# Optimization experiments

Measured on AMD Instinct MI355X. Metric: run time of the kernel, lower is better.

The kernel has to match this reference:

```python
import jax, jax.numpy as jnp
import numpy as np

EMB = 384
H = 6
D = 64
B = 256
T = 256


def setup_inputs() -> dict:
    key = jax.random.key(0)
    ks = jax.random.split(key, 6)
    s = 1.0 / np.sqrt(EMB)
    return {
        "x": jax.random.normal(ks[0], (B, T, EMB), dtype=jnp.float32),
        "wq": jax.random.normal(ks[1], (H, EMB, D), dtype=jnp.float32) * s,
        "wk": jax.random.normal(ks[2], (H, EMB, D), dtype=jnp.float32) * s,
        "wv": jax.random.normal(ks[3], (H, EMB, D), dtype=jnp.float32) * s,
        "w_proj": jax.random.normal(ks[4], (H * D, EMB), dtype=jnp.float32) * s,
        "b_proj": jax.random.normal(ks[5], (EMB,), dtype=jnp.float32) * 0.01,
    }


def reference(x, wq, wk, wv, w_proj, b_proj):
    # x: [B, T, E]; per-head projections stacked over H (dropout in eval mode)
    q = jnp.einsum("bte,hed->bhtd", x, wq)
    k = jnp.einsum("bte,hed->bhtd", x, wk)
    v = jnp.einsum("bte,hed->bhtd", x, wv)
    scale = q.shape[-1] ** -0.5
    scores = jnp.einsum("bhqd,bhkd->bhqk", q, k) * scale  # [B,H,T,T]
    tq = q.shape[2]
    causal = jnp.tril(jnp.ones((tq, tq), dtype=bool))
    scores = jnp.where(causal, scores, -jnp.inf)
    att = jax.nn.softmax(scores, axis=-1)
    out = jnp.einsum("bhqk,bhkd->bhqd", att, v)  # [B,H,T,D]
    out = out.transpose(0, 2, 1, 3).reshape(x.shape[0], tq, -1)  # concat heads
    return out @ w_proj + b_proj
```

## Files before the change

kernel.cpp:

```cpp
#include <hip/hip_runtime.h>
#include <hip/hip_bf16.h>


#define Bn 256
#define Tn 256
#define En 384
#define Hn 6
#define Dn 64

typedef __bf16 bf16x8 __attribute__((ext_vector_type(8)));
typedef float f32x4 __attribute__((ext_vector_type(4)));
typedef unsigned short u16x8 __attribute__((ext_vector_type(8)));

static __device__ __forceinline__ unsigned short f2bf(float f) {
    unsigned int u = __builtin_bit_cast(unsigned int, f);
    u += 0x7fffu + ((u >> 16) & 1u);
    return (unsigned short)(u >> 16);
}

static __device__ __forceinline__ f32x4 mfma16(bf16x8 a, bf16x8 b, f32x4 c) {
    return __builtin_amdgcn_mfma_f32_16x16x32_bf16(a, b, c, 0, 0, 0);
}

static __device__ __forceinline__ void glds16(const unsigned short* g, unsigned short* l) {
    __builtin_amdgcn_global_load_lds(
        (const __attribute__((address_space(1))) unsigned int*)g,
        (__attribute__((address_space(3))) unsigned int*)l, 16, 0, 0);
}

__global__ __launch_bounds__(256) void prep_kernel(
    const float* __restrict__ wq, const float* __restrict__ wk,
    const float* __restrict__ wv, const float* __restrict__ wp,
    unsigned short* __restrict__ wt, unsigned short* __restrict__ wpt) {
    const int NW = 3 * Hn * Dn * En;
    const int NP = En * En;
    int idx = blockIdx.x * 256 + threadIdx.x;
    if (idx < NW) {
        int e = idx % En;
        int d = (idx / En) % Dn;
        int h = (idx / (En * Dn)) % Hn;
        int t = idx / (En * Dn * Hn);
        const float* src = (t == 0) ? wq : (t == 1) ? wk : wv;
        wt[idx] = f2bf(src[(h * En + e) * Dn + d]);
    } else if (idx < NW + NP) {
        int j = idx - NW;
        int k = j % En;
        int n = j / En;
        wpt[j] = f2bf(wp[k * En + n]);
    }
}

__global__ __launch_bounds__(256) void xcast_kernel(
    const float* __restrict__ x, unsigned short* __restrict__ xb) {
    size_t i = ((size_t)blockIdx.x * 256 + threadIdx.x) * 8;
    float4 f0 = *(const float4*)(x + i);
    float4 f1 = *(const float4*)(x + i + 4);
    u16x8 p;
    p[0] = f2bf(f0.x); p[1] = f2bf(f0.y); p[2] = f2bf(f0.z); p[3] = f2bf(f0.w);
    p[4] = f2bf(f1.x); p[5] = f2bf(f1.y); p[6] = f2bf(f1.z); p[7] = f2bf(f1.w);
    *(u16x8*)(xb + i) = p;
}

__global__ __launch_bounds__(256) void qkv_gemm(
    const unsigned short* __restrict__ xb, const unsigned short* __restrict__ wt,
    unsigned short* __restrict__ Qo, unsigned short* __restrict__ Ko,
    unsigned short* __restrict__ Vt) {
    __shared__ unsigned short As[2][128][64];
    __shared__ unsigned short Bs[2][192][64];

    const int bid = blockIdx.x;
    const int swz = (bid & 7) * 384 + (bid >> 3);
    const int h = swz % Hn;
    const int m0 = (swz / Hn) * 128;

    const int tid = threadIdx.x;
    const int wave = tid >> 6, lane = tid & 63;
    const int quad = lane >> 4, l16 = lane & 15;
    const int mw = (wave >> 1) * 64, nw = (wave & 1) * 96;

    f32x4 acc[4][6];
#pragma unroll
    for (int i = 0; i < 4; ++i)
#pragma unroll
        for (int j = 0; j < 6; ++j) acc[i][j] = (f32x4){0.f, 0.f, 0.f, 0.f};

    const int lr = lane >> 3;
    const int js = (lane & 7) ^ lr;

    const unsigned short* ga[4];
#pragma unroll
    for (int i = 0; i < 4; ++i)
        ga[i] = xb + (size_t)(m0 + wave * 32 + i * 8 + lr) * En + js * 8;
    const unsigned short* gb[6];
#pragma unroll
    for (int i = 0; i < 6; ++i) {
        int n = wave * 48 + i * 8 + lr;
        gb[i] = wt + (size_t)(((n >> 6) * Hn + h) * Dn + (n & 63)) * En + js * 8;
    }

#define QKV_STAGE(buf, koff)                                              \
    do {                                                                  \
        _Pragma("unroll") for (int i = 0; i < 4; ++i)                     \
            glds16(ga[i] + (koff), &As[buf][wave * 32 + i * 8][0]);       \
        _Pragma("unroll") for (int i = 0; i < 6; ++i)                     \
            glds16(gb[i] + (koff), &Bs[buf][wave * 48 + i * 8][0]);       \
    } while (0)

    QKV_STAGE(0, 0);
    QKV_STAGE(1, 64);

#pragma unroll
    for (int kb = 0; kb < 6; ++kb) {
        if (kb < 5) asm volatile("s_waitcnt vmcnt(10)" ::: "memory");
        else        asm volatile("s_waitcnt vmcnt(0)" ::: "memory");
        __builtin_amdgcn_s_barrier();

        const int cur = kb & 1;
#pragma unroll
        for (int ks = 0; ks < 2; ++ks) {
            bf16x8 a[4], b[6];
            const int ps = ((ks * 4 + quad) ^ (l16 & 7)) * 8;
#pragma unroll
            for (int mi = 0; mi < 4; ++mi)
                a[mi] = *(const bf16x8*)&As[cur][mw + mi * 16 + l16][ps];
#pragma unroll
            for (int ni = 0; ni < 6; ++ni)
                b[ni] = *(const bf16x8*)&Bs[cur][nw + ni * 16 + l16][ps];
#pragma unroll
            for (int mi = 0; mi < 4; ++mi)
#pragma unroll
                for (int ni = 0; ni < 6; ++ni) acc[mi][ni] = mfma16(a[mi], b[ni], acc[mi][ni]);
        }

        if (kb < 4) {
            __builtin_amdgcn_s_barrier();
            QKV_STAGE(cur, (kb + 2) * 64);
        }
    }
#undef QKV_STAGE

    const int b = m0 >> 8, tbase = m0 & 255;
    unsigned short* qkbase[2] = {
        Qo + (size_t)((b * Hn + h) * Tn) * Dn,
        Ko + (size_t)((b * Hn + h) * Tn) * Dn };
    unsigned short* vdst = Vt + (size_t)((b * Hn + h) * Dn) * Tn;
#pragma unroll
    for (int ni = 0; ni < 6; ++ni) {
        const int ng = nw + ni * 16;
        const int tensor = ng >> 6;
        const int d = (ng & 63) + l16;
        if (tensor < 2) {
            unsigned short* dst = qkbase[tensor];
#pragma unroll
            for (int mi = 0; mi < 4; ++mi)
#pragma unroll
                for (int r = 0; r < 4; ++r) {
                    int t = tbase + mw + mi * 16 + quad * 4 + r;
                    dst[t * Dn + d] = f2bf(acc[mi][ni][r]);
                }
        } else {
#pragma unroll
            for (int mi = 0; mi < 4; ++mi) {
                int t0 = tbase + mw + mi * 16 + quad * 4;
                ushort4 pk;
                pk.x = f2bf(acc[mi][ni][0]);
                pk.y = f2bf(acc[mi][ni][1]);
                pk.z = f2bf(acc[mi][ni][2]);
                pk.w = f2bf(acc[mi][ni][3]);
                *(ushort4*)&vdst[d * Tn + t0] = pk;
            }
        }
    }
}

__global__ __launch_bounds__(256) void attn_kernel(
    const unsigned short* __restrict__ Q, const unsigned short* __restrict__ K,
    const unsigned short* __restrict__ Vt, unsigned short* __restrict__ attout) {
    __shared__ unsigned short Kt[256][64];
    __shared__ unsigned short Vl[64][256];
    __shared__ unsigned short P[4][16][72];

    const int h = blockIdx.x, b = blockIdx.y;
    const unsigned short* Qb = Q + (size_t)((b * Hn + h) * Tn) * Dn;
    const unsigned short* Kb = K + (size_t)((b * Hn + h) * Tn) * Dn;
    const unsigned short* Vb = Vt + (size_t)((b * Hn + h) * Dn) * Tn;

    const int tid = threadIdx.x;
    const int wave = tid >> 6, lane = tid & 63;
    const int quad = lane >> 4, l16 = lane & 15;

    {
        const unsigned short* kg = Kb + (size_t)(lane >> 3) * Dn + ((lane & 7) ^ (lane >> 3)) * 8;
#pragma unroll
        for (int i = 0; i < 8; ++i) {
            const int c = wave * 8 + i;
            glds16(kg + (size_t)c * 8 * Dn, &Kt[c * 8][0]);
        }
#pragma unroll
        for (int i = 0; i < 8; ++i) {
            const int c = wave * 8 + i;
            const int d = c * 2 + (lane >> 5);
            const int j = (lane & 31) ^ (d & 7);
            glds16(Vb + (size_t)d * Tn + j * 8, &Vl[c * 2][0]);
        }
    }
    __syncthreads();

    const float cexp = 0.125f * 1.44269504f;
    const int grp[4] = {wave, 7 - wave, 8 + wave, 15 - wave};

    for (int gi = 0; gi < 4; ++gi) {
        const int g = grp[gi];
        const int q0 = g * 16;

        bf16x8 aq[2];
#pragma unroll
        for (int ks = 0; ks < 2; ++ks)
            aq[ks] = *(const bf16x8*)&Qb[(q0 + l16) * Dn + ks * 32 + quad * 8];

        f32x4 O[4];
#pragma unroll
        for (int i = 0; i < 4; ++i) O[i] = (f32x4){0.f, 0.f, 0.f, 0.f};
        float rsum[4] = {0.f, 0.f, 0.f, 0.f};

        const int ktmax = g >> 2;
        for (int kt = 0; kt <= ktmax; ++kt) {
            f32x4 S[4];
#pragma unroll
            for (int i = 0; i < 4; ++i) S[i] = (f32x4){0.f, 0.f, 0.f, 0.f};
#pragma unroll
            for (int ks = 0; ks < 2; ++ks)
#pragma unroll
                for (int ni = 0; ni < 4; ++ni) {
                    bf16x8 bk = *(const bf16x8*)
                        &Kt[kt * 64 + ni * 16 + l16][(((ks * 4 + quad) ^ (l16 & 7)) * 8)];
                    S[ni] = mfma16(aq[ks], bk, S[ni]);
                }

#pragma unroll
            for (int ni = 0; ni < 4; ++ni)
#pragma unroll
                for (int r = 0; r < 4; ++r) {
                    int col = kt * 64 + ni * 16 + l16;
                    float p = exp2f(S[ni][r] * cexp);
                    p = (col > q0 + quad * 4 + r) ? 0.f : p;
                    rsum[r] += p;
                    P[wave][quad * 4 + r][ni * 16 + l16] = f2bf(p);
                }

#pragma unroll
            for (int ks = 0; ks < 2; ++ks) {
                bf16x8 ap = *(const bf16x8*)&P[wave][l16][ks * 32 + quad * 8];
#pragma unroll
                for (int ni = 0; ni < 4; ++ni) {
                    bf16x8 bv = *(const bf16x8*)
                        &Vl[ni * 16 + l16][(((kt * 8 + ks * 4 + quad) ^ (l16 & 7)) * 8)];
                    O[ni] = mfma16(ap, bv, O[ni]);
                }
            }
        }

#pragma unroll
        for (int r = 0; r < 4; ++r) {
            float s = rsum[r];
            s += __shfl_xor(s, 1);
            s += __shfl_xor(s, 2);
            s += __shfl_xor(s, 4);
            s += __shfl_xor(s, 8);
            rsum[r] = s;
        }

#pragma unroll
        for (int r = 0; r < 4; ++r) {
            float inv = 1.0f / rsum[r];
#pragma unroll
            for (int ni = 0; ni < 4; ++ni)
                P[wave][quad * 4 + r][ni * 16 + l16] = f2bf(O[ni][r] * inv);
        }
        const int row = lane >> 2;
        const int colc = (lane & 3) * 16;
        unsigned short* dst = attout + (size_t)(b * Tn + q0 + row) * (Hn * Dn) + h * Dn + colc;
        *(uint4*)dst = *(const uint4*)&P[wave][row][colc];
        *(uint4*)(dst + 8) = *(const uint4*)&P[wave][row][colc + 8];
    }
}

__global__ __launch_bounds__(256) void proj_gemm(
    const unsigned short* __restrict__ attout, const unsigned short* __restrict__ wpt,
    const float* __restrict__ bproj, float* __restrict__ out) {
    __shared__ unsigned short As[2][128][64];
    __shared__ unsigned short Bs[2][128][64];

    const int bid = blockIdx.x;
    const int swz = (bid & 7) * 192 + (bid >> 3);
    const int n0 = (swz % 3) * 128;
    const int m0 = (swz / 3) * 128;

    const int tid = threadIdx.x;
    const int wave = tid >> 6, lane = tid & 63;
    const int quad = lane >> 4, l16 = lane & 15;
    const int mw = (wave >> 1) * 64, nw = (wave & 1) * 64;

    f32x4 acc[4][4];
#pragma unroll
    for (int i = 0; i < 4; ++i)
#pragma unroll
        for (int j = 0; j < 4; ++j) acc[i][j] = (f32x4){0.f, 0.f, 0.f, 0.f};

    const int lr = lane >> 3;
    const int js = (lane & 7) ^ lr;

    const unsigned short* ga[4];
    const unsigned short* gb[4];
#pragma unroll
    for (int i = 0; i < 4; ++i) {
        ga[i] = attout + (size_t)(m0 + wave * 32 + i * 8 + lr) * En + js * 8;
        gb[i] = wpt + (size_t)(n0 + wave * 32 + i * 8 + lr) * En + js * 8;
    }

#define PROJ_STAGE(buf, koff)                                             \
    do {                                                                  \
        _Pragma("unroll") for (int i = 0; i < 4; ++i)                     \
            glds16(ga[i] + (koff), &As[buf][wave * 32 + i * 8][0]);       \
        _Pragma("unroll") for (int i = 0; i < 4; ++i)                     \
            glds16(gb[i] + (koff), &Bs[buf][wave * 32 + i * 8][0]);       \
    } while (0)

    PROJ_STAGE(0, 0);
    PROJ_STAGE(1, 64);

#pragma unroll
    for (int kb = 0; kb < 6; ++kb) {
        if (kb < 5) asm volatile("s_waitcnt vmcnt(8)" ::: "memory");
        else        asm volatile("s_waitcnt vmcnt(0)" ::: "memory");
        __builtin_amdgcn_s_barrier();

        const int cur = kb & 1;
#pragma unroll
        for (int ks = 0; ks < 2; ++ks) {
            bf16x8 a[4], bb[4];
            const int ps = ((ks * 4 + quad) ^ (l16 & 7)) * 8;
#pragma unroll
            for (int mi = 0; mi < 4; ++mi)
                a[mi] = *(const bf16x8*)&As[cur][mw + mi * 16 + l16][ps];
#pragma unroll
            for (int ni = 0; ni < 4; ++ni)
                bb[ni] = *(const bf16x8*)&Bs[cur][nw + ni * 16 + l16][ps];
#pragma unroll
            for (int mi = 0; mi < 4; ++mi)
#pragma unroll
                for (int ni = 0; ni < 4; ++ni) acc[mi][ni] = mfma16(a[mi], bb[ni], acc[mi][ni]);
        }

        if (kb < 4) {
            __builtin_amdgcn_s_barrier();
            PROJ_STAGE(cur, (kb + 2) * 64);
        }
    }
#undef PROJ_STAGE

#pragma unroll
    for (int mi = 0; mi < 4; ++mi)
#pragma unroll
        for (int ni = 0; ni < 4; ++ni)
#pragma unroll
            for (int r = 0; r < 4; ++r) {
                int row = m0 + mw + mi * 16 + quad * 4 + r;
                int col = n0 + nw + ni * 16 + l16;
                out[(size_t)row * En + col] = acc[mi][ni][r] + bproj[col];
            }
}

extern "C" void kernel_launch(void* const* d_in, const int* in_sizes, int n_in,
                              void* d_out, int out_size, void* d_ws, size_t ws_size,
                              hipStream_t stream) {
    const float* x  = (const float*)d_in[0];
    const float* wq = (const float*)d_in[1];
    const float* wk = (const float*)d_in[2];
    const float* wv = (const float*)d_in[3];
    const float* wp = (const float*)d_in[4];
    const float* bp = (const float*)d_in[5];
    float* out = (float*)d_out;

    char* ws = (char*)d_ws;
    const size_t WT_OFF  = 0;
    const size_t WPT_OFF = WT_OFF + 884736;
    const size_t Q_OFF   = WPT_OFF + 294912;
    const size_t K_OFF   = Q_OFF + 50331648ull;
    const size_t VT_OFF  = K_OFF + 50331648ull;
    const size_t XB_OFF  = VT_OFF + 50331648ull;

    unsigned short* wt   = (unsigned short*)(ws + WT_OFF);
    unsigned short* wpt  = (unsigned short*)(ws + WPT_OFF);
    unsigned short* Qd   = (unsigned short*)(ws + Q_OFF);
    unsigned short* Kd   = (unsigned short*)(ws + K_OFF);
    unsigned short* Vtd  = (unsigned short*)(ws + VT_OFF);
    unsigned short* xbd  = (unsigned short*)(ws + XB_OFF);
    unsigned short* ao   = xbd;

    prep_kernel<<<2304, 256, 0, stream>>>(wq, wk, wv, wp, wt, wpt);
    xcast_kernel<<<12288, 256, 0, stream>>>(x, xbd);
    qkv_gemm<<<3072, 256, 0, stream>>>(xbd, wt, Qd, Kd, Vtd);
    attn_kernel<<<dim3(Hn, Bn), 256, 0, stream>>>(Qd, Kd, Vtd, ao);
    proj_gemm<<<1536, 256, 0, stream>>>(ao, wpt, bp, out);
}
```

Before: 349.2 us.

## Merge prep and cast kernels, add MFMA priority hints, hoist Q loads

Combines the weight-prep and x-cast kernels into one launch to remove a kernel boundary. Wraps the MFMA inner loops in the GEMM and attention kernels with s_setprio so those waves get higher issue priority. Loads all four Q fragments per wave before the barrier, so the global loads overlap with the K/V LDS fill. Keeping the fragments live raises register pressure, and the fused launch mixes two unrelated workloads in one grid.

After: 344.9 us. Within noise of the previous version (-1.2%).

```diff
diff --git a/kernel.cpp b/kernel.cpp
--- a/kernel.cpp
+++ b/kernel.cpp
@@ -28,37 +28,39 @@
         (__attribute__((address_space(3))) unsigned int*)l, 16, 0, 0);
 }
 
-__global__ __launch_bounds__(256) void prep_kernel(
+__global__ __launch_bounds__(256) void prep_xcast_kernel(
     const float* __restrict__ wq, const float* __restrict__ wk,
     const float* __restrict__ wv, const float* __restrict__ wp,
-    unsigned short* __restrict__ wt, unsigned short* __restrict__ wpt) {
-    const int NW = 3 * Hn * Dn * En;
-    const int NP = En * En;
-    int idx = blockIdx.x * 256 + threadIdx.x;
-    if (idx < NW) {
-        int e = idx % En;
-        int d = (idx / En) % Dn;
-        int h = (idx / (En * Dn)) % Hn;
-        int t = idx / (En * Dn * Hn);
-        const float* src = (t == 0) ? wq : (t == 1) ? wk : wv;
-        wt[idx] = f2bf(src[(h * En + e) * Dn + d]);
-    } else if (idx < NW + NP) {
-        int j = idx - NW;
-        int k = j % En;
-        int n = j / En;
-        wpt[j] = f2bf(wp[k * En + n]);
-    }
-}
-
-__global__ __launch_bounds__(256) void xcast_kernel(
-    const float* __restrict__ x, unsigned short* __restrict__ xb) {
-    size_t i = ((size_t)blockIdx.x * 256 + threadIdx.x) * 8;
-    float4 f0 = *(const float4*)(x + i);
-    float4 f1 = *(const float4*)(x + i + 4);
-    u16x8 p;
-    p[0] = f2bf(f0.x); p[1] = f2bf(f0.y); p[2] = f2bf(f0.z); p[3] = f2bf(f0.w);
-    p[4] = f2bf(f1.x); p[5] = f2bf(f1.y); p[6] = f2bf(f1.z); p[7] = f2bf(f1.w);
-    *(u16x8*)(xb + i) = p;
+    const float* __restrict__ x,
+    unsigned short* __restrict__ wt, unsigned short* __restrict__ wpt,
+    unsigned short* __restrict__ xb) {
+    const int bid = blockIdx.x;
+    if (bid < 12288) {
+        size_t i = ((size_t)bid * 256 + threadIdx.x) * 8;
+        float4 f0 = *(const float4*)(x + i);
+        float4 f1 = *(const float4*)(x + i + 4);
+        u16x8 p;
+        p[0] = f2bf(f0.x); p[1] = f2bf(f0.y); p[2] = f2bf(f0.z); p[3] = f2bf(f0.w);
+        p[4] = f2bf(f1.x); p[5] = f2bf(f1.y); p[6] = f2bf(f1.z); p[7] = f2bf(f1.w);
+        *(u16x8*)(xb + i) = p;
+    } else {
+        const int NW = 3 * Hn * Dn * En;
+        const int NP = En * En;
+        int idx = (bid - 12288) * 256 + threadIdx.x;
+        if (idx < NW) {
+            int e = idx % En;
+            int d = (idx / En) % Dn;
+            int h = (idx / (En * Dn)) % Hn;
+            int t = idx / (En * Dn * Hn);
+            const float* src = (t == 0) ? wq : (t == 1) ? wk : wv;
+            wt[idx] = f2bf(src[(h * En + e) * Dn + d]);
+        } else if (idx < NW + NP) {
+            int j = idx - NW;
+            int k = j % En;
+            int n = j / En;
+            wpt[j] = f2bf(wp[k * En + n]);
+        }
+    }
 }
 
 __global__ __launch_bounds__(256) void qkv_gemm(
@@ -116,6 +118,7 @@
         __builtin_amdgcn_s_barrier();
 
         const int cur = kb & 1;
+        __builtin_amdgcn_s_setprio(1);
 #pragma unroll
         for (int ks = 0; ks < 2; ++ks) {
             bf16x8 a[4], b[6];
@@ -131,6 +134,7 @@
 #pragma unroll
                 for (int ni = 0; ni < 6; ++ni) acc[mi][ni] = mfma16(a[mi], b[ni], acc[mi][ni]);
         }
+        __builtin_amdgcn_s_setprio(0);
 
         if (kb < 4) {
             __builtin_amdgcn_s_barrier();
@@ -189,6 +193,8 @@
     const int wave = tid >> 6, lane = tid & 63;
     const int quad = lane >> 4, l16 = lane & 15;
 
+    const int grp[4] = {wave, 7 - wave, 8 + wave, 15 - wave};
+
     {
         const unsigned short* kg = Kb + (size_t)(lane >> 3) * Dn + ((lane & 7) ^ (lane >> 3)) * 8;
 #pragma unroll
@@ -204,20 +210,25 @@
             glds16(Vb + (size_t)d * Tn + j * 8, &Vl[c * 2][0]);
         }
     }
+
+    bf16x8 aq[4][2];
+#pragma unroll
+    for (int gi = 0; gi < 4; ++gi) {
+        const int q0 = grp[gi] * 16;
+#pragma unroll
+        for (int ks = 0; ks < 2; ++ks)
+            aq[gi][ks] = *(const bf16x8*)&Qb[(q0 + l16) * Dn + ks * 32 + quad * 8];
+    }
+
     __syncthreads();
 
     const float cexp = 0.125f * 1.44269504f;
-    const int grp[4] = {wave, 7 - wave, 8 + wave, 15 - wave};
-
+
+#pragma unroll
     for (int gi = 0; gi < 4; ++gi) {
         const int g = grp[gi];
         const int q0 = g * 16;
 
-        bf16x8 aq[2];
-#pragma unroll
-        for (int ks = 0; ks < 2; ++ks)
-            aq[ks] = *(const bf16x8*)&Qb[(q0 + l16) * Dn + ks * 32 + quad * 8];
-
         f32x4 O[4];
 #pragma unroll
         for (int i = 0; i < 4; ++i) O[i] = (f32x4){0.f, 0.f, 0.f, 0.f};
@@ -228,14 +239,16 @@
             f32x4 S[4];
 #pragma unroll
             for (int i = 0; i < 4; ++i) S[i] = (f32x4){0.f, 0.f, 0.f, 0.f};
+            __builtin_amdgcn_s_setprio(1);
 #pragma unroll
             for (int ks = 0; ks < 2; ++ks)
 #pragma unroll
                 for (int ni = 0; ni < 4; ++ni) {
                     bf16x8 bk = *(const bf16x8*)
                         &Kt[kt * 64 + ni * 16 + l16][(((ks * 4 + quad) ^ (l16 & 7)) * 8)];
-                    S[ni] = mfma16(aq[ks], bk, S[ni]);
+                    S[ni] = mfma16(aq[gi][ks], bk, S[ni]);
                 }
+            __builtin_amdgcn_s_setprio(0);
 
 #pragma unroll
             for (int ni = 0; ni < 4; ++ni)
@@ -248,6 +261,7 @@
                     P[wave][quad * 4 + r][ni * 16 + l16] = f2bf(p);
                 }
 
+            __builtin_amdgcn_s_setprio(1);
 #pragma unroll
             for (int ks = 0; ks < 2; ++ks) {
                 bf16x8 ap = *(const bf16x8*)&P[wave][l16][ks * 32 + quad * 8];
@@ -258,6 +272,7 @@
                     O[ni] = mfma16(ap, bv, O[ni]);
                 }
             }
+            __builtin_amdgcn_s_setprio(0);
         }
 
 #pragma unroll
@@ -336,6 +351,7 @@
         __builtin_amdgcn_s_barrier();
 
         const int cur = kb & 1;
+        __builtin_amdgcn_s_setprio(1);
 #pragma unroll
         for (int ks = 0; ks < 2; ++ks) {
             bf16x8 a[4], bb[4];
@@ -351,6 +367,7 @@
 #pragma unroll
                 for (int ni = 0; ni < 4; ++ni) acc[mi][ni] = mfma16(a[mi], bb[ni], acc[mi][ni]);
         }
+        __builtin_amdgcn_s_setprio(0);
 
         if (kb < 4) {
             __builtin_amdgcn_s_barrier();
@@ -398,8 +415,7 @@
     unsigned short* xbd  = (unsigned short*)(ws + XB_OFF);
     unsigned short* ao   = xbd;
 
-    prep_kernel<<<2304, 256, 0, stream>>>(wq, wk, wv, wp, wt, wpt);
-    xcast_kernel<<<12288, 256, 0, stream>>>(x, xbd);
+    prep_xcast_kernel<<<14592, 256, 0, stream>>>(wq, wk, wv, wp, x, wt, wpt, xbd);
     qkv_gemm<<<3072, 256, 0, stream>>>(xbd, wt, Qd, Kd, Vtd);
     attn_kernel<<<dim3(Hn, Bn), 256, 0, stream>>>(Qd, Kd, Vtd, ao);
     proj_gemm<<<1536, 256, 0, stream>>>(ao, wpt, bp, out);
```
